# Optimization experiments

Measured on AMD Instinct MI355X. Metric: run time of the kernel, lower is better.

## Reference

```python
import jax, jax.numpy as jnp
import numpy as np

NUM_CLASSES = 21
TOP_K = 200
VAR0, VAR1 = 0.1, 0.2
CONF_THRESH = 0.01
NMS_THRESH = 0.45
NUM_PRIORS = 3000
BATCH = 256


def _decode(loc, priors):
    # loc, priors: [P, 4] (cx, cy, w, h) -> corner boxes [P, 4]
    cxcy = priors[:, :2] + loc[:, :2] * VAR0 * priors[:, 2:]
    wh = priors[:, 2:] * jnp.exp(loc[:, 2:] * VAR1)
    return jnp.concatenate([cxcy - wh * 0.5, cxcy + wh * 0.5], axis=1)


def _iou_one_vs_all(box, boxes):
    # box [4], boxes [P,4] corner form
    lt = jnp.maximum(box[:2], boxes[:, :2])
    rb = jnp.minimum(box[2:], boxes[:, 2:])
    wh = jnp.clip(rb - lt, 0.0)
    inter = wh[:, 0] * wh[:, 1]
    area1 = (box[2] - box[0]) * (box[3] - box[1])
    area2 = (boxes[:, 2] - boxes[:, 0]) * (boxes[:, 3] - boxes[:, 1])
    return inter / (area1 + area2 - inter)


def _nms_one_class(boxes, scores):
    # boxes [P,4], scores [P] -> [TOP_K, 5] rows of (score, x1, y1, x2, y2)
    neg_inf = jnp.array(-jnp.inf, boxes.dtype)
    sc0 = jnp.where(scores > CONF_THRESH, scores, neg_inf)

    def step(sc, _):
        i = jnp.argmax(sc)
        s = sc[i]
        b = boxes[i]
        valid = s > CONF_THRESH
        iou = _iou_one_vs_all(b, boxes)
        sc = jnp.where(iou > NMS_THRESH, neg_inf, sc).at[i].set(neg_inf)
        row = jnp.where(valid, jnp.concatenate([s[None], b]), jnp.zeros(5, boxes.dtype))
        return sc, row

    _, rows = jax.lax.scan(step, sc0, None, length=TOP_K)
    return rows


def setup_inputs() -> dict:
    key = jax.random.key(0)
    k1, k2, k3 = jax.random.split(key, 3)
    loc_data = jax.random.normal(k1, (BATCH, NUM_PRIORS, 4), dtype=jnp.float32)
    conf_data = jax.random.uniform(k2, (BATCH, NUM_PRIORS, NUM_CLASSES), dtype=jnp.float32)
    pr = jax.random.uniform(k3, (NUM_PRIORS, 4), dtype=jnp.float32)
    # centers in [0,1], widths/heights in [0.05, 0.5]
    priors = jnp.concatenate([pr[:, :2], 0.05 + 0.45 * pr[:, 2:]], axis=1)
    return {"loc_data": loc_data, "conf_data": conf_data, "priors": priors}


def reference(loc_data, conf_data, priors):
    # decode per image: [B, P, 4]
    decoded = jax.vmap(lambda l: _decode(l, priors))(loc_data)
    # class-major scores, skipping background class 0: [B, C-1, P]
    cls_scores = jnp.transpose(conf_data, (0, 2, 1))[:, 1:, :]
    per_bc = jax.vmap(jax.vmap(_nms_one_class, in_axes=(None, 0)),
                      in_axes=(0, 0))(decoded, cls_scores)  # [B, C-1, TOP_K, 5]
    bg = jnp.zeros((loc_data.shape[0], 1, TOP_K, 5), loc_data.dtype)
    return jnp.concatenate([bg, per_bc], axis=1)  # [B, C, TOP_K, 5]
```

## Files before the change

### kernel.cpp

```cpp
#include <hip/hip_runtime.h>
#include <math.h>


#define NCLS 21
#define TOPK 200
#define NPRI 3000
#define ELTS 47
#define CONF_T 0.01f
#define MHI 0.45f
#define MLO 1.490116119384765625e-08f
#define CAP 256
#define NBUCK 256
#define NUSED 224
#define BITS_BASE 0x3C000000u
#define BSHIFT 18

__device__ __forceinline__ float rdlf(float v, int l) {
  return __int_as_float(__builtin_amdgcn_readlane(__float_as_int(v), l));
}

__device__ __forceinline__ bool iou_sup(const float4 k, const float a,
                                        const float4 b, const float carea) {
  float ltx = fmaxf(k.x, b.x), lty = fmaxf(k.y, b.y);
  float rbx = fminf(k.z, b.z), rby = fminf(k.w, b.w);
  float iw = fmaxf(rbx - ltx, 0.0f), ih = fmaxf(rby - lty, 0.0f);
  float inter = iw * ih;
  float uni = (a + carea) - inter;
  return fmaf(-MLO, uni, fmaf(-MHI, uni, inter)) > 0.0f;
}

__global__ void decode_kernel(const float* __restrict__ loc,
                              const float* __restrict__ priors,
                              float4* __restrict__ wsbox,
                              float* __restrict__ out) {
  const int b = blockIdx.x;
  float* o0 = out + (size_t)b * NCLS * TOPK * 5;
  for (int i = threadIdx.x; i < TOPK * 5; i += 256) o0[i] = 0.0f;
  for (int j = threadIdx.x; j < NPRI; j += 256) {
    const float4 l4 = *(const float4*)(loc + ((size_t)b * NPRI + j) * 4);
    const float4 p  = *(const float4*)(priors + (size_t)j * 4);
    float cx = p.x + (l4.x * 0.1f) * p.z;
    float cy = p.y + (l4.y * 0.1f) * p.w;
    float bw = p.z * expf(l4.z * 0.2f);
    float bh = p.w * expf(l4.w * 0.2f);
    wsbox[(size_t)b * NPRI + j] = make_float4(cx - bw * 0.5f, cy - bh * 0.5f,
                                              cx + bw * 0.5f, cy + bh * 0.5f);
  }
}

__global__ __launch_bounds__(128, 5) void ssd_nms_kernel(
    const float* __restrict__ conf, const float4* __restrict__ wsbox,
    float* __restrict__ out, int nbatch) {
  const int blk = blockIdx.x;
  int b, g;
  if ((nbatch & 7) == 0) {
    const int rest = blk >> 3;
    g = rest % 10;
    b = ((rest / 10) << 3) | (blk & 7);
  } else {
    b = blk / 10;
    g = blk % 10;
  }
  const int tid  = threadIdx.x;
  const int lane = tid & 63;
  const int w    = tid >> 6;
  const int c    = 1 + g * 2 + w;

  __shared__ unsigned long long skey[2][CAP];
  __shared__ unsigned int hist[2][NBUCK / 2];
  __shared__ float4 kbox[2][TOPK];
  __shared__ float  karr[2][TOPK];
  __shared__ float  kscore[2][TOPK];

  for (int i = lane; i < NBUCK / 2; i += 64) hist[w][i] = 0u;

  const float* myF = conf + (size_t)b * NPRI * NCLS + c;

#pragma unroll 4
  for (int k = 0; k < ELTS; ++k) {
    const int j = k * 64 + lane;
    unsigned int bits = 0u;
    if (j < NPRI) {
      float s = myF[(size_t)j * NCLS];
      bits = (s > CONF_T) ? __float_as_uint(s) : 0u;
    }
    if (bits) {
      unsigned int bu = (bits - BITS_BASE) >> BSHIFT;
      atomicAdd(&hist[w][bu >> 1], 1u << ((bu & 1) * 16));
    }
  }

  float* obase = out + ((size_t)b * NCLS + c) * (TOPK * 5);
  const float4* mybox = wsbox + (size_t)b * NPRI;
  int nk = 0;
  int cutHiB = NUSED;

  while (nk < TOPK && cutHiB > 0) {
    int sl = 0;
#pragma unroll
    for (int t = 0; t < 4; ++t) {
      int bu = lane * 4 + t;
      if (bu < cutHiB) sl += (int)((hist[w][bu >> 1] >> ((bu & 1) * 16)) & 0xFFFFu);
    }
    int suf = sl;
#pragma unroll
    for (int d = 1; d < 64; d <<= 1) {
      int v = __shfl_down(suf, d, 64);
      if (lane + d < 64) suf += v;
    }
    unsigned long long m = __ballot(suf <= CAP);
    int Ls = (m != 0ull) ? __builtin_ctzll(m) : 63;
    int cutLoB = Ls * 4;
    if (cutLoB >= cutHiB) cutLoB = (cutHiB - 1) & ~3;
    const unsigned int loBits = BITS_BASE + ((unsigned)cutLoB << BSHIFT);
    const unsigned int hiBits = BITS_BASE + ((unsigned)cutHiB << BSHIFT);

#pragma unroll
    for (int t = 0; t < CAP / 64; ++t) skey[w][t * 64 + lane] = 0ull;
    int base = 0;
#pragma unroll 2
    for (int k = 0; k < ELTS; ++k) {
      const int j = k * 64 + lane;
      unsigned int bits = 0u;
      if (j < NPRI) {
        float s = myF[(size_t)j * NCLS];
        bits = (s > CONF_T) ? __float_as_uint(s) : 0u;
      }
      bool sel = (bits >= loBits) && (bits < hiBits);
      unsigned long long bm = __ballot(sel);
      if (sel) {
        int pos = base + (int)__popcll(bm & ((1ull << lane) - 1ull));
        if (pos < CAP)
          skey[w][pos] = ((unsigned long long)bits << 12) | (unsigned)(4095 - j);
      }
      base += (int)__popcll(bm);
    }
    int Nc = (base > CAP) ? CAP : base;

    if (Nc > 0) {
      unsigned long long* sk = &skey[w][0];
      for (int kk = 2; kk <= CAP; kk <<= 1) {
        for (int jj = kk >> 1; jj > 0; jj >>= 1) {
#pragma unroll
          for (int t = 0; t < CAP / 64; ++t) {
            int i = t * 64 + lane;
            int ixj = i ^ jj;
            if (ixj > i) {
              unsigned long long a = sk[i], d = sk[ixj];
              bool up = (i & kk) == 0;
              bool swp = up ? (a < d) : (a > d);
              if (swp) { sk[i] = d; sk[ixj] = a; }
            }
          }
          __threadfence_block();
        }
      }

      for (int p0 = 0; p0 < Nc && nk < TOPK; p0 += 64) {
        const int p = p0 + lane;
        const bool valid = p < Nc;
        unsigned long long key = valid ? sk[p] : 0ull;
        unsigned int bits = (unsigned int)(key >> 12);
        int j = 4095 - (int)(key & 4095ull);
        float4 bx = mybox[valid ? j : 0];
        float carea = (bx.z - bx.x) * (bx.w - bx.y);

        unsigned long long smask = __ballot(!valid);
        int s = 0;
        for (; s + 3 < nk; s += 4) {
          float4 k0 = kbox[w][s];     float a0 = karr[w][s];
          float4 k1 = kbox[w][s + 1]; float a1 = karr[w][s + 1];
          float4 k2 = kbox[w][s + 2]; float a2 = karr[w][s + 2];
          float4 k3 = kbox[w][s + 3]; float a3 = karr[w][s + 3];
          smask |= __ballot(iou_sup(k0, a0, bx, carea));
          smask |= __ballot(iou_sup(k1, a1, bx, carea));
          smask |= __ballot(iou_sup(k2, a2, bx, carea));
          smask |= __ballot(iou_sup(k3, a3, bx, carea));
          if (smask == ~0ull) { s = nk; break; }
        }
        for (; s < nk; ++s) {
          float4 k0 = kbox[w][s]; float a0 = karr[w][s];
          smask |= __ballot(iou_sup(k0, a0, bx, carea));
        }

        unsigned long long M = ~smask;
        int nCnt = 0;
        float nx1 = 0, ny1 = 0, nx2 = 0, ny2 = 0, nar = 0;

        while (M && nk < TOPK) {
          int ls = (int)__builtin_ctzll(M);
          M &= M - 1ull;
          float sx1 = rdlf(bx.x, ls), sy1 = rdlf(bx.y, ls);
          float sx2 = rdlf(bx.z, ls), sy2 = rdlf(bx.w, ls);
          float sar = rdlf(carea, ls);
          unsigned int sbits =
              (unsigned int)__builtin_amdgcn_readlane((int)bits, ls);

          bool s_sup = false;
          if (lane < nCnt) {
            float ltx = fmaxf(nx1, sx1), lty = fmaxf(ny1, sy1);
            float rbx = fminf(nx2, sx2), rby = fminf(ny2, sy2);
            float iw = fmaxf(rbx - ltx, 0.0f), ih = fmaxf(rby - lty, 0.0f);
            float inter = iw * ih;
            float uni = (nar + sar) - inter;
            s_sup = fmaf(-MLO, uni, fmaf(-MHI, uni, inter)) > 0.0f;
          }
          if (__ballot(s_sup) != 0ull) continue;

          if (lane == nCnt) { nx1 = sx1; ny1 = sy1; nx2 = sx2; ny2 = sy2; nar = sar; }
          if (lane == 0) {
            kbox[w][nk]   = make_float4(sx1, sy1, sx2, sy2);
            karr[w][nk]   = sar;
            kscore[w][nk] = __uint_as_float(sbits);
          }
          ++nCnt;
          ++nk;
        }
      }
    }
    cutHiB = cutLoB;
  }

  const float* kbf = (const float*)&kbox[w][0];
  for (int i = lane; i < TOPK * 5; i += 64) {
    int r = i / 5;
    int col = i - r * 5;
    float v = 0.0f;
    if (r < nk) v = (col == 0) ? kscore[w][r] : kbf[r * 4 + (col - 1)];
    obase[i] = v;
  }
}

extern "C" void kernel_launch(void* const* d_in, const int* in_sizes, int n_in,
                              void* d_out, int out_size, void* d_ws, size_t ws_size,
                              hipStream_t stream) {
  const float* loc    = (const float*)d_in[0];
  const float* conf   = (const float*)d_in[1];
  const float* priors = (const float*)d_in[2];
  float* out = (float*)d_out;
  float4* wsbox = (float4*)d_ws;

  const int batch = in_sizes[0] / (NPRI * 4);
  hipLaunchKernelGGL(decode_kernel, dim3(batch), dim3(256), 0, stream,
                     loc, priors, wsbox, out);
  hipLaunchKernelGGL(ssd_nms_kernel, dim3(batch * 10), dim3(128), 0, stream,
                     conf, wsbox, out, batch);
}
```

Before: 515.5 us.

## Split each class NMS across two cooperating waves per block

Each block of 128 threads now handles one (image, class) pair instead of two pairs with one wave each. The two waves share the histogram, candidate compaction (via a shared atomic counter), bitonic sort and suppression tests, and then resolve survivors in sequence through a shared keep count. This halves the serial per-class work on each wave and doubles the grid, at the cost of many more block barriers. It also drops the batch-interleaved block mapping and raises the occupancy hint in launch bounds.

```diff
diff --git a/kernel.cpp b/kernel.cpp
--- a/kernel.cpp
+++ b/kernel.cpp
@@ -27,6 +27,45 @@
   float inter = iw * ih;
   float uni = (a + carea) - inter;
   return fmaf(-MLO, uni, fmaf(-MHI, uni, inter)) > 0.0f;
+}
+
+__device__ __forceinline__ int resolve_tile(
+    unsigned long long smask, const float4 bx, const float carea,
+    const unsigned int bits, const int lane, int nk,
+    float4* kbox, float* karr, float* kscore) {
+  unsigned long long M = ~smask;
+  int nCnt = 0;
+  float nx1 = 0, ny1 = 0, nx2 = 0, ny2 = 0, nar = 0;
+  while (M && nk < TOPK) {
+    int ls = (int)__builtin_ctzll(M);
+    M &= M - 1ull;
+    float sx1 = rdlf(bx.x, ls), sy1 = rdlf(bx.y, ls);
+    float sx2 = rdlf(bx.z, ls), sy2 = rdlf(bx.w, ls);
+    float sar = rdlf(carea, ls);
+    unsigned int sbits =
+        (unsigned int)__builtin_amdgcn_readlane((int)bits, ls);
+
+    bool s_sup = false;
+    if (lane < nCnt) {
+      float ltx = fmaxf(nx1, sx1), lty = fmaxf(ny1, sy1);
+      float rbx = fminf(nx2, sx2), rby = fminf(ny2, sy2);
+      float iw = fmaxf(rbx - ltx, 0.0f), ih = fmaxf(rby - lty, 0.0f);
+      float inter = iw * ih;
+      float uni = (nar + sar) - inter;
+      s_sup = fmaf(-MLO, uni, fmaf(-MHI, uni, inter)) > 0.0f;
+    }
+    if (__ballot(s_sup) != 0ull) continue;
+
+    if (lane == nCnt) { nx1 = sx1; ny1 = sy1; nx2 = sx2; ny2 = sy2; nar = sar; }
+    if (lane == 0) {
+      kbox[nk]   = make_float4(sx1, sy1, sx2, sy2);
+      karr[nk]   = sar;
+      kscore[nk] = __uint_as_float(sbits);
+    }
+    ++nCnt;
+    ++nk;
+  }
+  return nk;
 }
 
 __global__ void decode_kernel(const float* __restrict__ loc,
@@ -48,36 +87,31 @@
   }
 }
 
-__global__ __launch_bounds__(128, 5) void ssd_nms_kernel(
+__global__ __launch_bounds__(128, 8) void ssd_nms_kernel(
     const float* __restrict__ conf, const float4* __restrict__ wsbox,
-    float* __restrict__ out, int nbatch) {
-  const int blk = blockIdx.x;
-  int b, g;
-  if ((nbatch & 7) == 0) {
-    const int rest = blk >> 3;
-    g = rest % 10;
-    b = ((rest / 10) << 3) | (blk & 7);
-  } else {
-    b = blk / 10;
-    g = blk % 10;
-  }
+    float* __restrict__ out) {
+  const int blk  = blockIdx.x;
+  const int b    = blk / 20;
+  const int c    = 1 + blk % 20;
   const int tid  = threadIdx.x;
   const int lane = tid & 63;
   const int w    = tid >> 6;
-  const int c    = 1 + g * 2 + w;
-
-  __shared__ unsigned long long skey[2][CAP];
-  __shared__ unsigned int hist[2][NBUCK / 2];
-  __shared__ float4 kbox[2][TOPK];
-  __shared__ float  karr[2][TOPK];
-  __shared__ float  kscore[2][TOPK];
-
-  for (int i = lane; i < NBUCK / 2; i += 64) hist[w][i] = 0u;
+
+  __shared__ unsigned long long skey[CAP];
+  __shared__ unsigned int hist[NBUCK / 2];
+  __shared__ float4 kbox[TOPK];
+  __shared__ float  karr[TOPK];
+  __shared__ float  kscore[TOPK];
+  __shared__ int sh_nk;
+  __shared__ int sh_ctr;
+
+  for (int i = tid; i < NBUCK / 2; i += 128) hist[i] = 0u;
+  if (tid == 0) sh_nk = 0;
+  __syncthreads();
 
   const float* myF = conf + (size_t)b * NPRI * NCLS + c;
 
-#pragma unroll 4
-  for (int k = 0; k < ELTS; ++k) {
+  for (int k = w; k < ELTS; k += 2) {
     const int j = k * 64 + lane;
     unsigned int bits = 0u;
     if (j < NPRI) {
@@ -86,21 +120,23 @@
     }
     if (bits) {
       unsigned int bu = (bits - BITS_BASE) >> BSHIFT;
-      atomicAdd(&hist[w][bu >> 1], 1u << ((bu & 1) * 16));
-    }
-  }
+      atomicAdd(&hist[bu >> 1], 1u << ((bu & 1) * 16));
+    }
+  }
+  __syncthreads();
 
   float* obase = out + ((size_t)b * NCLS + c) * (TOPK * 5);
   const float4* mybox = wsbox + (size_t)b * NPRI;
-  int nk = 0;
   int cutHiB = NUSED;
 
-  while (nk < TOPK && cutHiB > 0) {
+  for (;;) {
+    if (sh_nk >= TOPK || cutHiB <= 0) break;
+
     int sl = 0;
 #pragma unroll
     for (int t = 0; t < 4; ++t) {
       int bu = lane * 4 + t;
-      if (bu < cutHiB) sl += (int)((hist[w][bu >> 1] >> ((bu & 1) * 16)) & 0xFFFFu);
+      if (bu < cutHiB) sl += (int)((hist[bu >> 1] >> ((bu & 1) * 16)) & 0xFFFFu);
     }
     int suf = sl;
 #pragma unroll
@@ -115,11 +151,11 @@
     const unsigned int loBits = BITS_BASE + ((unsigned)cutLoB << BSHIFT);
     const unsigned int hiBits = BITS_BASE + ((unsigned)cutHiB << BSHIFT);
 
-#pragma unroll
-    for (int t = 0; t < CAP / 64; ++t) skey[w][t * 64 + lane] = 0ull;
-    int base = 0;
-#pragma unroll 2
-    for (int k = 0; k < ELTS; ++k) {
+    if (tid == 0) sh_ctr = 0;
+    for (int t = tid; t < CAP; t += 128) skey[t] = 0ull;
+    __syncthreads();
+
+    for (int k = w; k < ELTS; k += 2) {
       const int j = k * 64 + lane;
       unsigned int bits = 0u;
       if (j < NPRI) {
@@ -128,38 +164,43 @@
       }
       bool sel = (bits >= loBits) && (bits < hiBits);
       unsigned long long bm = __ballot(sel);
+      int cnt = (int)__popcll(bm);
+      int wb = 0;
+      if (lane == 0 && cnt) wb = atomicAdd(&sh_ctr, cnt);
+      wb = __builtin_amdgcn_readfirstlane(wb);
       if (sel) {
-        int pos = base + (int)__popcll(bm & ((1ull << lane) - 1ull));
+        int pos = wb + (int)__popcll(bm & ((1ull << lane) - 1ull));
         if (pos < CAP)
-          skey[w][pos] = ((unsigned long long)bits << 12) | (unsigned)(4095 - j);
-      }
-      base += (int)__popcll(bm);
-    }
-    int Nc = (base > CAP) ? CAP : base;
+          skey[pos] = ((unsigned long long)bits << 12) | (unsigned)(4095 - j);
+      }
+    }
+    __syncthreads();
+    int Nc = sh_ctr;
+    if (Nc > CAP) Nc = CAP;
 
     if (Nc > 0) {
-      unsigned long long* sk = &skey[w][0];
       for (int kk = 2; kk <= CAP; kk <<= 1) {
         for (int jj = kk >> 1; jj > 0; jj >>= 1) {
-#pragma unroll
-          for (int t = 0; t < CAP / 64; ++t) {
-            int i = t * 64 + lane;
-            int ixj = i ^ jj;
-            if (ixj > i) {
-              unsigned long long a = sk[i], d = sk[ixj];
-              bool up = (i & kk) == 0;
-              bool swp = up ? (a < d) : (a > d);
-              if (swp) { sk[i] = d; sk[ixj] = a; }
-            }
-          }
-          __threadfence_block();
-        }
-      }
-
-      for (int p0 = 0; p0 < Nc && nk < TOPK; p0 += 64) {
-        const int p = p0 + lane;
+          if (jj == 128) __syncthreads();
+          int i = ((tid & ~(jj - 1)) << 1) | (tid & (jj - 1));
+          int ixj = i | jj;
+          unsigned long long a = skey[i], d = skey[ixj];
+          bool up = (i & kk) == 0;
+          if (up ? (a < d) : (a > d)) { skey[i] = d; skey[ixj] = a; }
+          if (jj == 128) __syncthreads();
+          else __threadfence_block();
+        }
+      }
+      __syncthreads();
+
+      for (int p0 = 0;; p0 += 128) {
+        if (p0 >= Nc) break;
+        const int nk0 = sh_nk;
+        if (nk0 >= TOPK) break;
+
+        const int p = p0 + w * 64 + lane;
         const bool valid = p < Nc;
-        unsigned long long key = valid ? sk[p] : 0ull;
+        unsigned long long key = valid ? skey[p] : 0ull;
         unsigned int bits = (unsigned int)(key >> 12);
         int j = 4095 - (int)(key & 4095ull);
         float4 bx = mybox[valid ? j : 0];
@@ -167,66 +208,48 @@
 
         unsigned long long smask = __ballot(!valid);
         int s = 0;
-        for (; s + 3 < nk; s += 4) {
-          float4 k0 = kbox[w][s];     float a0 = karr[w][s];
-          float4 k1 = kbox[w][s + 1]; float a1 = karr[w][s + 1];
-          float4 k2 = kbox[w][s + 2]; float a2 = karr[w][s + 2];
-          float4 k3 = kbox[w][s + 3]; float a3 = karr[w][s + 3];
+        for (; s + 3 < nk0; s += 4) {
+          float4 k0 = kbox[s];     float a0 = karr[s];
+          float4 k1 = kbox[s + 1]; float a1 = karr[s + 1];
+          float4 k2 = kbox[s + 2]; float a2 = karr[s + 2];
+          float4 k3 = kbox[s + 3]; float a3 = karr[s + 3];
           smask |= __ballot(iou_sup(k0, a0, bx, carea));
           smask |= __ballot(iou_sup(k1, a1, bx, carea));
           smask |= __ballot(iou_sup(k2, a2, bx, carea));
           smask |= __ballot(iou_sup(k3, a3, bx, carea));
-          if (smask == ~0ull) { s = nk; break; }
-        }
-        for (; s < nk; ++s) {
-          float4 k0 = kbox[w][s]; float a0 = karr[w][s];
-          smask |= __ballot(iou_sup(k0, a0, bx, carea));
-        }
-
-        unsigned long long M = ~smask;
-        int nCnt = 0;
-        float nx1 = 0, ny1 = 0, nx2 = 0, ny2 = 0, nar = 0;
-
-        while (M && nk < TOPK) {
-          int ls = (int)__builtin_ctzll(M);
-          M &= M - 1ull;
-          float sx1 = rdlf(bx.x, ls), sy1 = rdlf(bx.y, ls);
-          float sx2 = rdlf(bx.z, ls), sy2 = rdlf(bx.w, ls);
-          float sar = rdlf(carea, ls);
-          unsigned int sbits =
-              (unsigned int)__builtin_amdgcn_readlane((int)bits, ls);
-
-          bool s_sup = false;
-          if (lane < nCnt) {
-            float ltx = fmaxf(nx1, sx1), lty = fmaxf(ny1, sy1);
-            float rbx = fminf(nx2, sx2), rby = fminf(ny2, sy2);
-            float iw = fmaxf(rbx - ltx, 0.0f), ih = fmaxf(rby - lty, 0.0f);
-            float inter = iw * ih;
-            float uni = (nar + sar) - inter;
-            s_sup = fmaf(-MLO, uni, fmaf(-MHI, uni, inter)) > 0.0f;
-          }
-          if (__ballot(s_sup) != 0ull) continue;
-
-          if (lane == nCnt) { nx1 = sx1; ny1 = sy1; nx2 = sx2; ny2 = sy2; nar = sar; }
-          if (lane == 0) {
-            kbox[w][nk]   = make_float4(sx1, sy1, sx2, sy2);
-            karr[w][nk]   = sar;
-            kscore[w][nk] = __uint_as_float(sbits);
-          }
-          ++nCnt;
-          ++nk;
-        }
+          if (smask == ~0ull) { s = nk0; break; }
+        }
+        for (; s < nk0; ++s)
+          smask |= __ballot(iou_sup(kbox[s], karr[s], bx, carea));
+
+        if (w == 0) {
+          int nk = resolve_tile(smask, bx, carea, bits, lane, nk0,
+                                kbox, karr, kscore);
+          if (lane == 0) sh_nk = nk;
+        }
+        __syncthreads();
+        if (w == 1) {
+          const int nk1 = sh_nk;
+          for (int s2 = nk0; s2 < nk1; ++s2)
+            smask |= __ballot(iou_sup(kbox[s2], karr[s2], bx, carea));
+          int nk = resolve_tile(smask, bx, carea, bits, lane, nk1,
+                                kbox, karr, kscore);
+          if (lane == 0) sh_nk = nk;
+        }
+        __syncthreads();
       }
     }
     cutHiB = cutLoB;
   }
 
-  const float* kbf = (const float*)&kbox[w][0];
-  for (int i = lane; i < TOPK * 5; i += 64) {
+  __syncthreads();
+  const int nkf = sh_nk;
+  const float* kbf = (const float*)&kbox[0];
+  for (int i = tid; i < TOPK * 5; i += 128) {
     int r = i / 5;
     int col = i - r * 5;
     float v = 0.0f;
-    if (r < nk) v = (col == 0) ? kscore[w][r] : kbf[r * 4 + (col - 1)];
+    if (r < nkf) v = (col == 0) ? kscore[r] : kbf[r * 4 + (col - 1)];
     obase[i] = v;
   }
 }
@@ -243,6 +266,6 @@
   const int batch = in_sizes[0] / (NPRI * 4);
   hipLaunchKernelGGL(decode_kernel, dim3(batch), dim3(256), 0, stream,
                      loc, priors, wsbox, out);
-  hipLaunchKernelGGL(ssd_nms_kernel, dim3(batch * 10), dim3(128), 0, stream,
-                     conf, wsbox, out, batch);
-}
+  hipLaunchKernelGGL(ssd_nms_kernel, dim3(batch * 20), dim3(128), 0, stream,
+                     conf, wsbox, out);
+}
```

Result: slower. 551.4 us (+7.0%).
